# Kernel optimization log

Hardware: AMD Instinct MI355X
Metric: run time of the kernel (lower is better)

The kernel has to match this reference:

```python
import jax, jax.numpy as jnp
import numpy as np

B, S, I, H, O = 4096, 512, 28, 128, 28

def setup_inputs() -> dict:
    key = jax.random.key(0)
    ks = jax.random.split(key, 7)
    s = lambda fan_in: 1.0 / np.sqrt(fan_in)
    return {
        "x":    jax.random.normal(ks[0], (B, S, I), dtype=jnp.float32),
        "W_ih": jax.random.uniform(ks[1], (I, H), jnp.float32, -s(I), s(I)),
        "b_ih": jax.random.uniform(ks[2], (H,),  jnp.float32, -s(I), s(I)),
        "W_hh": jax.random.uniform(ks[3], (H, H), jnp.float32, -s(H), s(H)),
        "b_hh": jax.random.uniform(ks[4], (H,),  jnp.float32, -s(H), s(H)),
        "W_ho": jax.random.uniform(ks[5], (H, O), jnp.float32, -s(H), s(H)),
        "b_ho": jax.random.uniform(ks[6], (O,),  jnp.float32, -s(H), s(H)),
    }

def reference(x, W_ih, b_ih, W_hh, b_hh, W_ho, b_ho):
    # Precompute input projections for all timesteps in one big GEMM: [B,S,H]
    xproj = jnp.einsum("bsi,ih->bsh", x, W_ih) + b_ih
    h0 = jnp.zeros((x.shape[0], W_hh.shape[0]), dtype=x.dtype)

    def step(h, xp_t):
        h = jnp.tanh(xp_t + h @ W_hh + b_hh)
        return h, None

    # scan over time axis: xproj transposed to [S,B,H]
    h_final, _ = jax.lax.scan(step, h0, jnp.swapaxes(xproj, 0, 1))
    return h_final @ W_ho + b_ho
```

## Files before the change

kernel.cpp:

```cpp
#include <hip/hip_runtime.h>
#include <stdint.h>

#define S_LEN 512
#define I_DIM 28
#define H_DIM 128
#define O_DIM 28
#define BT    16

typedef __attribute__((ext_vector_type(8))) short bf16x8;
typedef __attribute__((ext_vector_type(4))) float f32x4;

static __device__ __forceinline__ short f2bf(float f) {
    unsigned u = __float_as_uint(f);
    u = (u + 0x7fffu + ((u >> 16) & 1u)) >> 16;
    return (short)u;
}
static __device__ __forceinline__ float bf2f(unsigned short u) {
    return __uint_as_float(((unsigned)u) << 16);
}
static __device__ __forceinline__ unsigned cvt_pk(float a, float b) {
    unsigned r;
    asm("v_cvt_pk_bf16_f32 %0, %1, %2" : "=v"(r) : "v"(a), "v"(b));
    return r;
}
static __device__ __forceinline__ f32x4 pade_tanh4(f32x4 x) {
    f32x4 u = x * x;
    f32x4 n = __builtin_elementwise_fma(u, u + 105.0f, (f32x4)(945.0f)) * x;
    f32x4 d = __builtin_elementwise_fma(
                  u, __builtin_elementwise_fma(u, (f32x4)(15.0f), (f32x4)(420.0f)),
                  (f32x4)(945.0f));
    f32x4 r;
    r[0] = __builtin_amdgcn_rcpf(d[0]); r[1] = __builtin_amdgcn_rcpf(d[1]);
    r[2] = __builtin_amdgcn_rcpf(d[2]); r[3] = __builtin_amdgcn_rcpf(d[3]);
    f32x4 t = n * r;
    t = __builtin_elementwise_max(t, (f32x4)(-1.0f));
    t = __builtin_elementwise_min(t, (f32x4)(1.0f));
    return t;
}

__global__ __launch_bounds__(512, 1) void rnn_fused(
    const float* __restrict__ x,
    const float* __restrict__ W_ih, const float* __restrict__ b_ih,
    const float* __restrict__ W_hh, const float* __restrict__ b_hh,
    const float* __restrict__ W_ho, const float* __restrict__ b_ho,
    float* __restrict__ out)
{
    const int tid  = threadIdx.x;
    const int wave = tid >> 6;
    const int lane = tid & 63;
    const int l15  = lane & 15;
    const int lk   = lane >> 4;
    const int r0   = blockIdx.x * BT;

    __shared__ __align__(16) bf16x8 hx[2][4][64];
    __shared__ __align__(16) bf16x8 xring[16][64];

    bf16x8 Ahh0, Ahh1, Ahh2, Ahh3, Aih;
    f32x4  biasv;
    const int jA = 16 * wave + l15;
    #pragma unroll
    for (int e = 0; e < 8; ++e) {
        Ahh0[e] = f2bf(W_hh[(  0 + lk * 8 + e) * H_DIM + jA]);
        Ahh1[e] = f2bf(W_hh[( 32 + lk * 8 + e) * H_DIM + jA]);
        Ahh2[e] = f2bf(W_hh[( 64 + lk * 8 + e) * H_DIM + jA]);
        Ahh3[e] = f2bf(W_hh[( 96 + lk * 8 + e) * H_DIM + jA]);
        int i = lk * 8 + e;
        Aih[e] = (i < I_DIM) ? f2bf(W_ih[i * H_DIM + jA]) : (short)0;
    }
    #pragma unroll
    for (int r = 0; r < 4; ++r) {
        int jC = 16 * wave + lk * 4 + r;
        biasv[r] = b_ih[jC] + b_hh[jC];
    }

    const int wboff = (wave >> 1) * 1024
                    + ((2 * (wave & 1) + (lk >> 1)) * 16 + l15) * 16
                    + 8 * (lk & 1);

    ((uint2*)&hx[0][0][0])[tid] = make_uint2(0u, 0u);

    const bool hasHi = (lk < 3);
    const float* xbase = x + (size_t)(r0 + l15) * S_LEN * I_DIM + lk * 8;

    {
        const float* src = xbase + wave * I_DIM;
        float4 lo = *(const float4*)src;
        float4 hi = hasHi ? *(const float4*)(src + 4) : make_float4(0.f,0.f,0.f,0.f);
        union { bf16x8 v; unsigned u[4]; } fr;
        fr.u[0] = cvt_pk(lo.x, lo.y); fr.u[1] = cvt_pk(lo.z, lo.w);
        fr.u[2] = cvt_pk(hi.x, hi.y); fr.u[3] = cvt_pk(hi.z, hi.w);
        xring[wave][lane] = fr.v;
    }
    asm volatile("s_waitcnt lgkmcnt(0)" ::: "memory");
    __builtin_amdgcn_s_barrier();
    asm volatile("" ::: "memory");

    f32x4 xacc;
    {
        bf16x8 x0 = xring[0][lane];
        xacc = biasv;
        xacc = __builtin_amdgcn_mfma_f32_16x16x32_bf16(Aih, x0, xacc, 0, 0, 0);
    }

#define RSTEP(PAR, P)                                                          \
    {                                                                          \
        const bf16x8* hxp = &hx[PAR][0][0];                                    \
        bf16x8 b0 = hxp[0 * 64 + lane];                                        \
        bf16x8 b1 = hxp[1 * 64 + lane];                                        \
        bf16x8 b2 = hxp[2 * 64 + lane];                                        \
        bf16x8 b3 = hxp[3 * 64 + lane];                                        \
        bf16x8 xn = xring[(t8 + P + 1) & 15][lane];  \
        if (P == 0 && doPf) {                                                  \
            const float* src = xbase + (size_t)tf * I_DIM;                     \
            pf_lo = *(const float4*)src;                                       \
            if (hasHi) pf_hi = *(const float4*)(src + 4);                      \
        }                                                                      \
        f32x4 a = xacc;                                                        \
        a = __builtin_amdgcn_mfma_f32_16x16x32_bf16(Ahh0, b0, a, 0, 0, 0);     \
        a = __builtin_amdgcn_mfma_f32_16x16x32_bf16(Ahh1, b1, a, 0, 0, 0);     \
        f32x4 c = {0.f, 0.f, 0.f, 0.f};                                        \
        c = __builtin_amdgcn_mfma_f32_16x16x32_bf16(Ahh2, b2, c, 0, 0, 0);     \
        c = __builtin_amdgcn_mfma_f32_16x16x32_bf16(Ahh3, b3, c, 0, 0, 0);     \
        if (P == 2 && doPf) {                                                  \
            union { bf16x8 v; unsigned u[4]; } fr;                             \
            fr.u[0] = cvt_pk(pf_lo.x, pf_lo.y); fr.u[1] = cvt_pk(pf_lo.z, pf_lo.w); \
            fr.u[2] = cvt_pk(pf_hi.x, pf_hi.y); fr.u[3] = cvt_pk(pf_hi.z, pf_hi.w); \
            xring[tf & 15][lane] = fr.v;                                       \
        }                                                                      \
        f32x4 s = a + c;                                                       \
                  \
        xacc = biasv;                                                          \
        xacc = __builtin_amdgcn_mfma_f32_16x16x32_bf16(Aih, xn, xacc, 0, 0, 0);\
        f32x4 h = pade_tanh4(s);                                               \
        uint2 wv;                                                              \
        wv.x = cvt_pk(h[0], h[1]); wv.y = cvt_pk(h[2], h[3]);                  \
        *(uint2*)((char*)&hx[(PAR) ^ 1][0][0] + wboff) = wv;                   \
        asm volatile("s_waitcnt lgkmcnt(0)" ::: "memory");                     \
        __builtin_amdgcn_s_barrier();                                          \
        asm volatile("" ::: "memory");                                        \
    }

    for (int t8 = 0; t8 < S_LEN; t8 += 8) {
        const int tf   = t8 + 8 + wave;
        const bool doPf = (tf < S_LEN);
        float4 pf_lo = make_float4(0.f,0.f,0.f,0.f), pf_hi = pf_lo;
        RSTEP(0, 0)
        RSTEP(1, 1)
        RSTEP(0, 2)
        RSTEP(1, 3)
        RSTEP(0, 4)
        RSTEP(1, 5)
        RSTEP(0, 6)
        RSTEP(1, 7)
    }
#undef RSTEP

    for (int idx = tid; idx < BT * O_DIM; idx += 512) {
        const int b = idx / O_DIM;
        const int o = idx - b * O_DIM;
        float sum = b_ho[o];
        const unsigned short* hb = (const unsigned short*)&hx[0][0][0];
        #pragma unroll 4
        for (int j = 0; j < H_DIM; ++j) {
            int slot = (j >> 5) * 64 + ((j >> 3) & 3) * 16 + b;
            sum += bf2f(hb[slot * 8 + (j & 7)]) * W_ho[j * O_DIM + o];
        }
        out[(size_t)(r0 + b) * O_DIM + o] = sum;
    }
}

extern "C" void kernel_launch(void* const* d_in, const int* in_sizes, int n_in,
                              void* d_out, int out_size, void* d_ws, size_t ws_size,
                              hipStream_t stream) {
    const float* x    = (const float*)d_in[0];
    const float* W_ih = (const float*)d_in[1];
    const float* b_ih = (const float*)d_in[2];
    const float* W_hh = (const float*)d_in[3];
    const float* b_hh = (const float*)d_in[4];
    const float* W_ho = (const float*)d_in[5];
    const float* b_ho = (const float*)d_in[6];
    const int B = in_sizes[0] / (S_LEN * I_DIM);
    rnn_fused<<<B / BT, 512, 0, stream>>>(x, W_ih, b_ih, W_hh, b_hh, W_ho, b_ho,
                                          (float*)d_out);
}
```

Measured before the change: 161.5 us.

## Replace LDS x ring buffer with per-wave register prefetch of input timesteps

Drops the shared-memory ring that staged bf16 input rows. Each wave now loads its own 8-timestep block of x from global memory into registers one block ahead, and converts it to bf16 fragments at the block boundary. This removes the LDS reads and writes of x from the per-step critical path. In exchange, every wave reads the same x data redundantly (8x global/L1 traffic), register pressure rises, and load latency must be hidden across an 8-step block.

```diff
diff --git a/kernel.cpp b/kernel.cpp
--- a/kernel.cpp
+++ b/kernel.cpp
@@ -53,7 +53,6 @@
     const int r0   = blockIdx.x * BT;
 
     __shared__ __align__(16) bf16x8 hx[2][4][64];
-    __shared__ __align__(16) bf16x8 xring[16][64];
 
     bf16x8 Ahh0, Ahh1, Ahh2, Ahh3, Aih;
     f32x4  biasv;
@@ -79,58 +78,64 @@
 
     ((uint2*)&hx[0][0][0])[tid] = make_uint2(0u, 0u);
 
-    const bool hasHi = (lk < 3);
     const float* xbase = x + (size_t)(r0 + l15) * S_LEN * I_DIM + lk * 8;
+    const int hioff = (lk < 3) ? 4 : 0;
 
-    {
-        const float* src = xbase + wave * I_DIM;
-        float4 lo = *(const float4*)src;
-        float4 hi = hasHi ? *(const float4*)(src + 4) : make_float4(0.f,0.f,0.f,0.f);
-        union { bf16x8 v; unsigned u[4]; } fr;
-        fr.u[0] = cvt_pk(lo.x, lo.y); fr.u[1] = cvt_pk(lo.z, lo.w);
-        fr.u[2] = cvt_pk(hi.x, hi.y); fr.u[3] = cvt_pk(hi.z, hi.w);
-        xring[wave][lane] = fr.v;
+    float4 rl0, rl1, rl2, rl3, rl4, rl5, rl6, rl7;
+    float4 rh0, rh1, rh2, rh3, rh4, rh5, rh6, rh7;
+    bf16x8 xf0, xf1, xf2, xf3, xf4, xf5, xf6, xf7;
+
+#define LOADG(T8)                                                              \
+    {                                                                          \
+        const float* g0 = xbase + (size_t)(T8) * I_DIM;                        \
+        const float* g1 = g0 + hioff;                                          \
+        rl0 = *(const float4*)(g0 + 0 * I_DIM); rh0 = *(const float4*)(g1 + 0 * I_DIM); \
+        rl1 = *(const float4*)(g0 + 1 * I_DIM); rh1 = *(const float4*)(g1 + 1 * I_DIM); \
+        rl2 = *(const float4*)(g0 + 2 * I_DIM); rh2 = *(const float4*)(g1 + 2 * I_DIM); \
+        rl3 = *(const float4*)(g0 + 3 * I_DIM); rh3 = *(const float4*)(g1 + 3 * I_DIM); \
+        rl4 = *(const float4*)(g0 + 4 * I_DIM); rh4 = *(const float4*)(g1 + 4 * I_DIM); \
+        rl5 = *(const float4*)(g0 + 5 * I_DIM); rh5 = *(const float4*)(g1 + 5 * I_DIM); \
+        rl6 = *(const float4*)(g0 + 6 * I_DIM); rh6 = *(const float4*)(g1 + 6 * I_DIM); \
+        rl7 = *(const float4*)(g0 + 7 * I_DIM); rh7 = *(const float4*)(g1 + 7 * I_DIM); \
     }
+
+#define CVT1(XF, RL, RH)                                                       \
+    {                                                                          \
+        union { bf16x8 v; unsigned u[4]; } fr_;                                \
+        fr_.u[0] = cvt_pk(RL.x, RL.y); fr_.u[1] = cvt_pk(RL.z, RL.w);          \
+        fr_.u[2] = cvt_pk(RH.x, RH.y); fr_.u[3] = cvt_pk(RH.z, RH.w);          \
+        XF = fr_.v;                                                            \
+    }
+
+    LOADG(0)
+    CVT1(xf0, rl0, rh0) CVT1(xf1, rl1, rh1) CVT1(xf2, rl2, rh2) CVT1(xf3, rl3, rh3)
+    CVT1(xf4, rl4, rh4) CVT1(xf5, rl5, rh5) CVT1(xf6, rl6, rh6) CVT1(xf7, rl7, rh7)
+    LOADG(8)
+
+    f32x4 xacc = biasv;
+    xacc = __builtin_amdgcn_mfma_f32_16x16x32_bf16(Aih, xf0, xacc, 0, 0, 0);
+
     asm volatile("s_waitcnt lgkmcnt(0)" ::: "memory");
     __builtin_amdgcn_s_barrier();
     asm volatile("" ::: "memory");
 
-    f32x4 xacc;
-    {
-        bf16x8 x0 = xring[0][lane];
-        xacc = biasv;
-        xacc = __builtin_amdgcn_mfma_f32_16x16x32_bf16(Aih, x0, xacc, 0, 0, 0);
-    }
-
-#define RSTEP(PAR, P)                                                          \
+#define RSTEP(PAR, XN)                                                         \
     {                                                                          \
         const bf16x8* hxp = &hx[PAR][0][0];                                    \
         bf16x8 b0 = hxp[0 * 64 + lane];                                        \
         bf16x8 b1 = hxp[1 * 64 + lane];                                        \
         bf16x8 b2 = hxp[2 * 64 + lane];                                        \
         bf16x8 b3 = hxp[3 * 64 + lane];                                        \
-        bf16x8 xn = xring[(t8 + P + 1) & 15][lane];  \
-        if (P == 0 && doPf) {                                                  \
-            const float* src = xbase + (size_t)tf * I_DIM;                     \
-            pf_lo = *(const float4*)src;                                       \
-            if (hasHi) pf_hi = *(const float4*)(src + 4);                      \
-        }                                                                      \
         f32x4 a = xacc;                                                        \
         a = __builtin_amdgcn_mfma_f32_16x16x32_bf16(Ahh0, b0, a, 0, 0, 0);     \
         a = __builtin_amdgcn_mfma_f32_16x16x32_bf16(Ahh1, b1, a, 0, 0, 0);     \
         f32x4 c = {0.f, 0.f, 0.f, 0.f};                                        \
         c = __builtin_amdgcn_mfma_f32_16x16x32_bf16(Ahh2, b2, c, 0, 0, 0);     \
         c = __builtin_amdgcn_mfma_f32_16x16x32_bf16(Ahh3, b3, c, 0, 0, 0);     \
-        if (P == 2 && doPf) {                                                  \
-            union { bf16x8 v; unsigned u[4]; } fr;                             \
-            fr.u[0] = cvt_pk(pf_lo.x, pf_lo.y); fr.u[1] = cvt_pk(pf_lo.z, pf_lo.w); \
-            fr.u[2] = cvt_pk(pf_hi.x, pf_hi.y); fr.u[3] = cvt_pk(pf_hi.z, pf_hi.w); \
-            xring[tf & 15][lane] = fr.v;                                       \
-        }                                                                      \
         f32x4 s = a + c;                                                       \
-                  \
+                     \
         xacc = biasv;                                                          \
-        xacc = __builtin_amdgcn_mfma_f32_16x16x32_bf16(Aih, xn, xacc, 0, 0, 0);\
+        xacc = __builtin_amdgcn_mfma_f32_16x16x32_bf16(Aih, XN, xacc, 0, 0, 0);\
         f32x4 h = pade_tanh4(s);                                               \
         uint2 wv;                                                              \
         wv.x = cvt_pk(h[0], h[1]); wv.y = cvt_pk(h[2], h[3]);                  \
@@ -141,19 +146,27 @@
     }
 
     for (int t8 = 0; t8 < S_LEN; t8 += 8) {
-        const int tf   = t8 + 8 + wave;
-        const bool doPf = (tf < S_LEN);
-        float4 pf_lo = make_float4(0.f,0.f,0.f,0.f), pf_hi = pf_lo;
-        RSTEP(0, 0)
-        RSTEP(1, 1)
-        RSTEP(0, 2)
-        RSTEP(1, 3)
-        RSTEP(0, 4)
-        RSTEP(1, 5)
-        RSTEP(0, 6)
-        RSTEP(1, 7)
+        RSTEP(0, xf1)
+        RSTEP(1, xf2)
+        RSTEP(0, xf3)
+        RSTEP(1, xf4)
+        RSTEP(0, xf5)
+        RSTEP(1, xf6)
+        RSTEP(0, xf7)
+        bf16x8 xf0n;
+        CVT1(xf0n, rl0, rh0)
+        RSTEP(1, xf0n)
+        if (t8 + 8 < S_LEN) {
+            xf0 = xf0n;
+            CVT1(xf1, rl1, rh1) CVT1(xf2, rl2, rh2) CVT1(xf3, rl3, rh3)
+            CVT1(xf4, rl4, rh4) CVT1(xf5, rl5, rh5) CVT1(xf6, rl6, rh6)
+            CVT1(xf7, rl7, rh7)
+            if (t8 + 16 < S_LEN) LOADG(t8 + 16)
+        }
     }
 #undef RSTEP
+#undef CVT1
+#undef LOADG
 
     for (int idx = tid; idx < BT * O_DIM; idx += 512) {
         const int b = idx / O_DIM;
```

New measurement: 300.7 us. 1.86x slower.
